# Performance work log

Measured on AMD Instinct MI355X. Metric: run time of the kernel, lower is better.

## Reference

```python
import jax, jax.numpy as jnp
import numpy as np

TEMP = 0.2
EPS = 1e-12  # F.normalize eps


def setup_inputs() -> dict:
    key = jax.random.key(0)
    k1, k2 = jax.random.split(key)
    l, B, K, D = 4, 64, 32, 128
    emb_i = jax.random.normal(k1, (l, B, K, D), dtype=jnp.float32)
    emb_j = jax.random.normal(k2, (l, B, K, D), dtype=jnp.float32)
    joint_valid = jnp.ones((B, K), dtype=jnp.float32)
    return {"emb_i": emb_i, "emb_j": emb_j, "joint_valid": joint_valid}


def _l2norm(x):
    n = jnp.sqrt(jnp.sum(x * x, axis=-1, keepdims=True))
    return x / jnp.maximum(n, EPS)


def reference(emb_i, emb_j, joint_valid):
    l, B, K, D = emb_i.shape
    N = B * K
    z_i = _l2norm(emb_i.reshape(l, N, D))
    z_j = _l2norm(emb_j.reshape(l, N, D))
    reps = jnp.concatenate([z_i, z_j], axis=1)              # (l, 2N, D), unit rows
    # cosine similarity of unit vectors == matmul
    sim = jnp.einsum('lnd,lmd->lnm', reps, reps)            # (l, 2N, 2N)
    idx = jnp.arange(N)
    pos = sim[:, idx, idx + N]                              # diag offset +N, (l, N)
    # note: original code uses the SAME +N offset diagonal for both ij and ji
    positives = jnp.concatenate([pos, pos], axis=1)         # (l, 2N)
    neg_mask = 1.0 - jnp.eye(2 * N, dtype=sim.dtype)        # (2N, 2N)
    denom = jnp.sum(neg_mask[None] * jnp.exp(sim / TEMP), axis=2)  # (l, 2N)
    loss_partial = -jnp.log(jnp.exp(positives / TEMP) / denom)    # (l, 2N)
    joints_mask = joint_valid.reshape(1, 1, B, K)
    all_num = jnp.sum(joint_valid)
    loss = jnp.sum(loss_partial.reshape(l, 2, B, K) * joints_mask) / (2.0 * all_num)
    return loss
```

## Files before the change

kernel.cpp:

```cpp
#include <hip/hip_runtime.h>
#include <hip/hip_bf16.h>

typedef __attribute__((ext_vector_type(8))) short short8;
typedef __attribute__((ext_vector_type(4))) float floatx4;

#define NROWS 4096
#define NHALF 2048
#define DDIM  128
#define LDST  136
#define SQRT_SCALE 2.6857914f
#define LN2 0.69314718056f

#define WS_PART_OFF 64
#define WS_DIAG_OFF 524352
#define WS_POS_OFF  540736
#define WS_Z_BYTE_OFF 2228480

__device__ inline unsigned short f2bf(float f) {
    unsigned u = __builtin_bit_cast(unsigned, f);
    u += 0x7fffu + ((u >> 16) & 1u);
    return (unsigned short)(u >> 16);
}

__global__ __launch_bounds__(256) void k_norm(const float* __restrict__ emb_i,
                                              const float* __restrict__ emb_j,
                                              const float* __restrict__ jv,
                                              float* __restrict__ wsf,
                                              unsigned short* __restrict__ z) {
    int bx = blockIdx.x, tid = threadIdx.x;
    if (bx == 4096) {
        __shared__ float sred[256];
        float s = 0.f;
        #pragma unroll
        for (int i = 0; i < 8; ++i) s += jv[tid + 256 * i];
        sred[tid] = s; __syncthreads();
        for (int off = 128; off > 0; off >>= 1) {
            if (tid < off) sred[tid] += sred[tid + off];
            __syncthreads();
        }
        if (tid == 0) wsf[1] = sred[0];
        return;
    }
    if (bx == 0 && tid == 0) { wsf[0] = 0.f; *(unsigned*)&wsf[2] = 0u; }

    int wave = tid >> 6, lane = tid & 63;
    int r = bx * 4 + wave;
    int l = r >> 12, n = r & 4095;
    const float* src = (n < NHALF) ? (emb_i + ((size_t)l * NHALF + n) * DDIM)
                                   : (emb_j + ((size_t)l * NHALF + (n - NHALF)) * DDIM);
    float2 v = *(const float2*)(src + lane * 2);
    float ss = v.x * v.x + v.y * v.y;
    #pragma unroll
    for (int off = 1; off < 64; off <<= 1) ss += __shfl_xor(ss, off);
    float inv = SQRT_SCALE / fmaxf(sqrtf(ss), 1e-12f);
    unsigned pack = ((unsigned)f2bf(v.y * inv) << 16) | (unsigned)f2bf(v.x * inv);
    *(unsigned*)(z + (size_t)r * DDIM + lane * 2) = pack;
}

__global__ __launch_bounds__(256) void k_sim(const unsigned short* __restrict__ z,
                                             float* __restrict__ part,
                                             float* __restrict__ diag,
                                             float* __restrict__ pos) {
    __shared__ __align__(16) unsigned short lds[128 * LDST];
    int bx = blockIdx.x, tid = threadIdx.x;
    int l = bx & 3, idx = bx >> 2;
    int J = (int)((sqrtf(8.f * (float)idx + 1.f) - 1.f) * 0.5f);
    while ((J + 1) * (J + 2) / 2 <= idx) ++J;
    while (J * (J + 1) / 2 > idx) --J;
    int I = idx - J * (J + 1) / 2;
    int wave = tid >> 6, lane = tid & 63, m = lane & 15, quad = lane >> 4;
    const unsigned short* zl = z + (size_t)l * NROWS * DDIM;
    int l4 = l * NROWS;
    int wr0 = I * 128 + wave * 32;
    int cg0 = J * 128;

    short8 a[2][4];
    #pragma unroll
    for (int rs = 0; rs < 2; ++rs) {
        const unsigned short* p = zl + (size_t)(wr0 + rs * 16 + m) * DDIM + quad * 8;
        #pragma unroll
        for (int kk = 0; kk < 4; ++kk) a[rs][kk] = *(const short8*)(p + kk * 32);
    }
    floatx4 rsum[2];
    #pragma unroll
    for (int rs = 0; rs < 2; ++rs) rsum[rs] = (floatx4){0.f, 0.f, 0.f, 0.f};
    float csum[8];
    #pragma unroll
    for (int g = 0; g < 8; ++g) csum[g] = 0.f;

    #pragma unroll
    for (int i = 0; i < 8; ++i) {
        int chunk = tid + 256 * i;
        int col = chunk >> 4, off = chunk & 15;
        uint4 d = *(const uint4*)(zl + (size_t)(cg0 + col) * DDIM + off * 8);
        *(uint4*)&lds[col * LDST + off * 8] = d;
    }
    __syncthreads();

    #pragma unroll
    for (int cs = 0; cs < 8; ++cs) {
        int ct = cg0 + cs * 16;
        const unsigned short* lp = &lds[(cs * 16 + m) * LDST + quad * 8];
        short8 b0 = *(const short8*)(lp);
        short8 b1 = *(const short8*)(lp + 32);
        short8 b2 = *(const short8*)(lp + 64);
        short8 b3 = *(const short8*)(lp + 96);
        #pragma unroll
        for (int rs = 0; rs < 2; ++rs) {
            floatx4 acc = (floatx4){0.f, 0.f, 0.f, 0.f};
            acc = __builtin_amdgcn_mfma_f32_16x16x32_bf16(a[rs][0], b0, acc, 0, 0, 0);
            acc = __builtin_amdgcn_mfma_f32_16x16x32_bf16(a[rs][1], b1, acc, 0, 0, 0);
            acc = __builtin_amdgcn_mfma_f32_16x16x32_bf16(a[rs][2], b2, acc, 0, 0, 0);
            acc = __builtin_amdgcn_mfma_f32_16x16x32_bf16(a[rs][3], b3, acc, 0, 0, 0);
            int rowbase = wr0 + rs * 16;
            bool isdiag = (ct == rowbase);
            bool ispos  = (ct == rowbase + 2048);
            if (isdiag || ispos) {
                int c = m - (quad << 2);
                if (c >= 0 && c < 4) {
                    float v = acc[c];
                    if (isdiag) diag[l4 + rowbase + m] = v;
                    else {
                        pos[l4 + rowbase + m] = v;
                        pos[l4 + rowbase + m + NHALF] = v;
                    }
                }
            }
            float t = 0.f;
            #pragma unroll
            for (int c = 0; c < 4; ++c) {
                float e = __builtin_amdgcn_exp2f(acc[c]);
                rsum[rs][c] += e;
                t += e;
            }
            csum[cs] += t;
        }
    }
    #pragma unroll
    for (int off = 1; off < 16; off <<= 1)
        #pragma unroll
        for (int rs = 0; rs < 2; ++rs)
            #pragma unroll
            for (int c = 0; c < 4; ++c)
                rsum[rs][c] += __shfl_xor(rsum[rs][c], off);
    float* plJ = part + (size_t)(l * 32 + J) * 4096;
    if (m == 0) {
        #pragma unroll
        for (int rs = 0; rs < 2; ++rs)
            #pragma unroll
            for (int c = 0; c < 4; ++c)
                plJ[wr0 + rs * 16 + quad * 4 + c] = rsum[rs][c];
    }
    if (I != J) {
        __syncthreads();
        float* cred = (float*)lds;
        #pragma unroll
        for (int g = 0; g < 8; ++g) {
            float v = csum[g];
            v += __shfl_xor(v, 16);
            v += __shfl_xor(v, 32);
            if (quad == 0) cred[wave * 128 + g * 16 + m] = v;
        }
        __syncthreads();
        if (tid < 128) {
            float s = cred[tid] + cred[tid + 128] + cred[tid + 256] + cred[tid + 384];
            part[(size_t)(l * 32 + I) * 4096 + cg0 + tid] = s;
        }
    }
}

__global__ __launch_bounds__(256) void k_loss(const float* __restrict__ jv,
                                              const float* __restrict__ part,
                                              const float* __restrict__ diag,
                                              const float* __restrict__ pos,
                                              float* __restrict__ wsf,
                                              float* __restrict__ out) {
    __shared__ float sred[256];
    int tid = threadIdx.x;
    int r = blockIdx.x * 256 + tid;
    int l = r >> 12, n = r & 4095;
    const float* pl = part + (size_t)l * 32 * 4096 + n;
    float s = 0.f;
    #pragma unroll
    for (int k = 0; k < 32; ++k) s += pl[(size_t)k * 4096];
    float denom = s - __builtin_amdgcn_exp2f(diag[r]);
    float contrib = LN2 * (__builtin_amdgcn_logf(denom) - pos[r]);
    float local = contrib * jv[n & (NHALF - 1)];
    sred[tid] = local; __syncthreads();
    for (int off = 128; off > 0; off >>= 1) {
        if (tid < off) sred[tid] += sred[tid + off];
        __syncthreads();
    }
    if (tid == 0) {
        atomicAdd(&wsf[0], sred[0]);
        __threadfence();
        unsigned c = atomicAdd((unsigned*)&wsf[2], 1u);
        if (c == 63) {
            float tot = atomicAdd(&wsf[0], 0.f);
            out[0] = tot / (2.f * wsf[1]);
        }
    }
}

extern "C" void kernel_launch(void* const* d_in, const int* in_sizes, int n_in,
                              void* d_out, int out_size, void* d_ws, size_t ws_size,
                              hipStream_t stream) {
    const float* emb_i = (const float*)d_in[0];
    const float* emb_j = (const float*)d_in[1];
    const float* jv    = (const float*)d_in[2];
    float* wsf  = (float*)d_ws;
    float* part = wsf + WS_PART_OFF;
    float* diag = wsf + WS_DIAG_OFF;
    float* pos  = wsf + WS_POS_OFF;
    unsigned short* z = (unsigned short*)((char*)d_ws + WS_Z_BYTE_OFF);
    float* out = (float*)d_out;

    k_norm <<<4097, 256, 0, stream>>>(emb_i, emb_j, jv, wsf, z);
    k_sim  <<<2112, 256, 0, stream>>>(z, part, diag, pos);
    k_loss <<<64,   256, 0, stream>>>(jv, part, diag, pos, wsf, out);
}
```

Before: 89.27 us.

## Make similarity kernel persistent with register-prefetched next tile

The similarity kernel now runs as a persistent grid of 512 blocks, each walking a strided list of 4-5 triangular tiles instead of launching one block per tile. While the current tile's MFMA and exp work runs, the next tile's column block is prefetched into registers and its row fragments are loaded, then written to LDS after the reduction. This hides global-load latency and reduces per-block launch and setup overhead. The cost is higher register pressure from the prefetch buffers, extra barriers per tile, and a tail imbalance because some blocks process one more tile than others.

Result: slower. 103.9 us (+16.3%).

```diff
diff --git a/kernel.cpp b/kernel.cpp
--- a/kernel.cpp
+++ b/kernel.cpp
@@ -20,6 +20,13 @@
     unsigned u = __builtin_bit_cast(unsigned, f);
     u += 0x7fffu + ((u >> 16) & 1u);
     return (unsigned short)(u >> 16);
+}
+
+__device__ inline void tilecoords(int idx, int& I, int& J) {
+    int j = (int)((sqrtf(8.f * (float)idx + 1.f) - 1.f) * 0.5f);
+    while ((j + 1) * (j + 2) / 2 <= idx) ++j;
+    while (j * (j + 1) / 2 > idx) --j;
+    J = j; I = idx - j * (j + 1) / 2;
 }
 
 __global__ __launch_bounds__(256) void k_norm(const float* __restrict__ emb_i,
@@ -62,110 +69,141 @@
                                              float* __restrict__ diag,
                                              float* __restrict__ pos) {
     __shared__ __align__(16) unsigned short lds[128 * LDST];
+    __shared__ float cred[4][128];
     int bx = blockIdx.x, tid = threadIdx.x;
-    int l = bx & 3, idx = bx >> 2;
-    int J = (int)((sqrtf(8.f * (float)idx + 1.f) - 1.f) * 0.5f);
-    while ((J + 1) * (J + 2) / 2 <= idx) ++J;
-    while (J * (J + 1) / 2 > idx) --J;
-    int I = idx - J * (J + 1) / 2;
+    int l = bx & 3, ppos = bx >> 2;
+    int nt = 4 + (ppos < 16);
     int wave = tid >> 6, lane = tid & 63, m = lane & 15, quad = lane >> 4;
     const unsigned short* zl = z + (size_t)l * NROWS * DDIM;
     int l4 = l * NROWS;
-    int wr0 = I * 128 + wave * 32;
-    int cg0 = J * 128;
+
+    int I, J;
+    tilecoords(ppos, I, J);
 
     short8 a[2][4];
     #pragma unroll
     for (int rs = 0; rs < 2; ++rs) {
-        const unsigned short* p = zl + (size_t)(wr0 + rs * 16 + m) * DDIM + quad * 8;
-        #pragma unroll
-        for (int kk = 0; kk < 4; ++kk) a[rs][kk] = *(const short8*)(p + kk * 32);
-    }
-    floatx4 rsum[2];
-    #pragma unroll
-    for (int rs = 0; rs < 2; ++rs) rsum[rs] = (floatx4){0.f, 0.f, 0.f, 0.f};
-    float csum[8];
-    #pragma unroll
-    for (int g = 0; g < 8; ++g) csum[g] = 0.f;
-
+        const unsigned short* pa = zl + (size_t)(I * 128 + wave * 32 + rs * 16 + m) * DDIM + quad * 8;
+        #pragma unroll
+        for (int kk = 0; kk < 4; ++kk) a[rs][kk] = *(const short8*)(pa + kk * 32);
+    }
     #pragma unroll
     for (int i = 0; i < 8; ++i) {
         int chunk = tid + 256 * i;
         int col = chunk >> 4, off = chunk & 15;
-        uint4 d = *(const uint4*)(zl + (size_t)(cg0 + col) * DDIM + off * 8);
+        uint4 d = *(const uint4*)(zl + (size_t)(J * 128 + col) * DDIM + off * 8);
         *(uint4*)&lds[col * LDST + off * 8] = d;
     }
     __syncthreads();
 
-    #pragma unroll
-    for (int cs = 0; cs < 8; ++cs) {
-        int ct = cg0 + cs * 16;
-        const unsigned short* lp = &lds[(cs * 16 + m) * LDST + quad * 8];
-        short8 b0 = *(const short8*)(lp);
-        short8 b1 = *(const short8*)(lp + 32);
-        short8 b2 = *(const short8*)(lp + 64);
-        short8 b3 = *(const short8*)(lp + 96);
+    for (int k = 0; k < nt; ++k) {
+        int nidx = ppos + (k + 1) * 128;
+        if (nidx >= 528) nidx = ppos;
+        int In, Jn;
+        tilecoords(nidx, In, Jn);
+        uint4 pf[8];
+        #pragma unroll
+        for (int i = 0; i < 8; ++i) {
+            int chunk = tid + 256 * i;
+            int col = chunk >> 4, off = chunk & 15;
+            pf[i] = *(const uint4*)(zl + (size_t)(Jn * 128 + col) * DDIM + off * 8);
+        }
+        short8 an[2][4];
         #pragma unroll
         for (int rs = 0; rs < 2; ++rs) {
-            floatx4 acc = (floatx4){0.f, 0.f, 0.f, 0.f};
-            acc = __builtin_amdgcn_mfma_f32_16x16x32_bf16(a[rs][0], b0, acc, 0, 0, 0);
-            acc = __builtin_amdgcn_mfma_f32_16x16x32_bf16(a[rs][1], b1, acc, 0, 0, 0);
-            acc = __builtin_amdgcn_mfma_f32_16x16x32_bf16(a[rs][2], b2, acc, 0, 0, 0);
-            acc = __builtin_amdgcn_mfma_f32_16x16x32_bf16(a[rs][3], b3, acc, 0, 0, 0);
-            int rowbase = wr0 + rs * 16;
-            bool isdiag = (ct == rowbase);
-            bool ispos  = (ct == rowbase + 2048);
-            if (isdiag || ispos) {
-                int c = m - (quad << 2);
-                if (c >= 0 && c < 4) {
-                    float v = acc[c];
-                    if (isdiag) diag[l4 + rowbase + m] = v;
-                    else {
-                        pos[l4 + rowbase + m] = v;
-                        pos[l4 + rowbase + m + NHALF] = v;
+            const unsigned short* pa = zl + (size_t)(In * 128 + wave * 32 + rs * 16 + m) * DDIM + quad * 8;
+            #pragma unroll
+            for (int kk = 0; kk < 4; ++kk) an[rs][kk] = *(const short8*)(pa + kk * 32);
+        }
+
+        int wr0 = I * 128 + wave * 32, cg0 = J * 128;
+        floatx4 rsum[2];
+        rsum[0] = (floatx4){0.f, 0.f, 0.f, 0.f};
+        rsum[1] = (floatx4){0.f, 0.f, 0.f, 0.f};
+        float csum[8];
+        #pragma unroll
+        for (int g = 0; g < 8; ++g) csum[g] = 0.f;
+
+        #pragma unroll
+        for (int cs = 0; cs < 8; ++cs) {
+            int ct = cg0 + cs * 16;
+            const unsigned short* lp = &lds[(cs * 16 + m) * LDST + quad * 8];
+            short8 b0 = *(const short8*)(lp);
+            short8 b1 = *(const short8*)(lp + 32);
+            short8 b2 = *(const short8*)(lp + 64);
+            short8 b3 = *(const short8*)(lp + 96);
+            #pragma unroll
+            for (int rs = 0; rs < 2; ++rs) {
+                floatx4 acc = (floatx4){0.f, 0.f, 0.f, 0.f};
+                acc = __builtin_amdgcn_mfma_f32_16x16x32_bf16(a[rs][0], b0, acc, 0, 0, 0);
+                acc = __builtin_amdgcn_mfma_f32_16x16x32_bf16(a[rs][1], b1, acc, 0, 0, 0);
+                acc = __builtin_amdgcn_mfma_f32_16x16x32_bf16(a[rs][2], b2, acc, 0, 0, 0);
+                acc = __builtin_amdgcn_mfma_f32_16x16x32_bf16(a[rs][3], b3, acc, 0, 0, 0);
+                int rowbase = wr0 + rs * 16;
+                bool isdiag = (ct == rowbase);
+                bool ispos  = (ct == rowbase + 2048);
+                if (isdiag || ispos) {
+                    int c = m - (quad << 2);
+                    if (c >= 0 && c < 4) {
+                        float v = acc[c];
+                        if (isdiag) diag[l4 + rowbase + m] = v;
+                        else {
+                            pos[l4 + rowbase + m] = v;
+                            pos[l4 + rowbase + m + NHALF] = v;
+                        }
                     }
                 }
+                float t = 0.f;
+                #pragma unroll
+                for (int c = 0; c < 4; ++c) {
+                    float e = __builtin_amdgcn_exp2f(acc[c]);
+                    rsum[rs][c] += e;
+                    t += e;
+                }
+                csum[cs] += t;
             }
-            float t = 0.f;
-            #pragma unroll
-            for (int c = 0; c < 4; ++c) {
-                float e = __builtin_amdgcn_exp2f(acc[c]);
-                rsum[rs][c] += e;
-                t += e;
+        }
+        #pragma unroll
+        for (int off = 1; off < 16; off <<= 1)
+            #pragma unroll
+            for (int rs = 0; rs < 2; ++rs)
+                #pragma unroll
+                for (int c = 0; c < 4; ++c)
+                    rsum[rs][c] += __shfl_xor(rsum[rs][c], off);
+        float* plJ = part + (size_t)(l * 32 + J) * 4096;
+        if (m == 0) {
+            #pragma unroll
+            for (int rs = 0; rs < 2; ++rs)
+                #pragma unroll
+                for (int c = 0; c < 4; ++c)
+                    plJ[wr0 + rs * 16 + quad * 4 + c] = rsum[rs][c];
+        }
+        if (I != J) {
+            #pragma unroll
+            for (int g = 0; g < 8; ++g) {
+                float v = csum[g];
+                v += __shfl_xor(v, 16);
+                v += __shfl_xor(v, 32);
+                if (quad == 0) cred[wave][g * 16 + m] = v;
             }
-            csum[cs] += t;
-        }
-    }
-    #pragma unroll
-    for (int off = 1; off < 16; off <<= 1)
+        }
+        __syncthreads();
+        if (I != J && tid < 128) {
+            float s = cred[0][tid] + cred[1][tid] + cred[2][tid] + cred[3][tid];
+            part[(size_t)(l * 32 + I) * 4096 + cg0 + tid] = s;
+        }
+        #pragma unroll
+        for (int i = 0; i < 8; ++i) {
+            int chunk = tid + 256 * i;
+            int col = chunk >> 4, off = chunk & 15;
+            *(uint4*)&lds[col * LDST + off * 8] = pf[i];
+        }
+        __syncthreads();
         #pragma unroll
         for (int rs = 0; rs < 2; ++rs)
             #pragma unroll
-            for (int c = 0; c < 4; ++c)
-                rsum[rs][c] += __shfl_xor(rsum[rs][c], off);
-    float* plJ = part + (size_t)(l * 32 + J) * 4096;
-    if (m == 0) {
-        #pragma unroll
-        for (int rs = 0; rs < 2; ++rs)
-            #pragma unroll
-            for (int c = 0; c < 4; ++c)
-                plJ[wr0 + rs * 16 + quad * 4 + c] = rsum[rs][c];
-    }
-    if (I != J) {
-        __syncthreads();
-        float* cred = (float*)lds;
-        #pragma unroll
-        for (int g = 0; g < 8; ++g) {
-            float v = csum[g];
-            v += __shfl_xor(v, 16);
-            v += __shfl_xor(v, 32);
-            if (quad == 0) cred[wave * 128 + g * 16 + m] = v;
-        }
-        __syncthreads();
-        if (tid < 128) {
-            float s = cred[tid] + cred[tid + 128] + cred[tid + 256] + cred[tid + 384];
-            part[(size_t)(l * 32 + I) * 4096 + cg0 + tid] = s;
-        }
+            for (int kk = 0; kk < 4; ++kk) a[rs][kk] = an[rs][kk];
+        I = In; J = Jn;
     }
 }
 
@@ -216,6 +254,6 @@
     float* out = (float*)d_out;
 
     k_norm <<<4097, 256, 0, stream>>>(emb_i, emb_j, jv, wsf, z);
-    k_sim  <<<2112, 256, 0, stream>>>(z, part, diag, pos);
+    k_sim  <<<512,  256, 0, stream>>>(z, part, diag, pos);
     k_loss <<<64,   256, 0, stream>>>(jv, part, diag, pos, wsf, out);
 }
```

## Process up to four column tiles per block to reuse row fragments

Applied to the files above, without the earlier changes.

The similarity kernel now walks a strip of up to four column tiles per block instead of one tile per block, cutting the grid from 2112 to 576 blocks. The A-row fragments stay in registers across the strip, and each next column tile is loaded into LDS after a barrier. This removes redundant A loads and per-block setup. In exchange it gives fewer blocks to hide latency, uneven work per block (one to four tiles), and B-tile loads that are serialized rather than overlapped with compute.

Measured after the change: 98.93 us. 1.11x slower.

```diff
diff --git a/kernel.cpp b/kernel.cpp
--- a/kernel.cpp
+++ b/kernel.cpp
@@ -62,110 +62,128 @@
                                              float* __restrict__ diag,
                                              float* __restrict__ pos) {
     __shared__ __align__(16) unsigned short lds[128 * LDST];
+    __shared__ float cred[4][128];
     int bx = blockIdx.x, tid = threadIdx.x;
-    int l = bx & 3, idx = bx >> 2;
-    int J = (int)((sqrtf(8.f * (float)idx + 1.f) - 1.f) * 0.5f);
-    while ((J + 1) * (J + 2) / 2 <= idx) ++J;
-    while (J * (J + 1) / 2 > idx) --J;
-    int I = idx - J * (J + 1) / 2;
+    int l = bx & 3, t = bx >> 2;
+    int cb = 0, cum = 0;
+    while (cb < 7) {
+        int n = 4 * cb + 4; if (n > 32) n = 32;
+        if (cum + n > t) break;
+        cum += n; ++cb;
+    }
+    int rb = t - cum;
+    int k0 = rb > 4 * cb ? rb : 4 * cb;
+    int k1 = 4 * cb + 3;
+
     int wave = tid >> 6, lane = tid & 63, m = lane & 15, quad = lane >> 4;
     const unsigned short* zl = z + (size_t)l * NROWS * DDIM;
     int l4 = l * NROWS;
-    int wr0 = I * 128 + wave * 32;
-    int cg0 = J * 128;
+    int wr0 = rb * 128 + wave * 32;
 
     short8 a[2][4];
     #pragma unroll
     for (int rs = 0; rs < 2; ++rs) {
-        const unsigned short* p = zl + (size_t)(wr0 + rs * 16 + m) * DDIM + quad * 8;
-        #pragma unroll
-        for (int kk = 0; kk < 4; ++kk) a[rs][kk] = *(const short8*)(p + kk * 32);
-    }
-    floatx4 rsum[2];
-    #pragma unroll
-    for (int rs = 0; rs < 2; ++rs) rsum[rs] = (floatx4){0.f, 0.f, 0.f, 0.f};
-    float csum[8];
-    #pragma unroll
-    for (int g = 0; g < 8; ++g) csum[g] = 0.f;
+        const unsigned short* pa = zl + (size_t)(wr0 + rs * 16 + m) * DDIM + quad * 8;
+        #pragma unroll
+        for (int kk = 0; kk < 4; ++kk) a[rs][kk] = *(const short8*)(pa + kk * 32);
+    }
 
     #pragma unroll
     for (int i = 0; i < 8; ++i) {
         int chunk = tid + 256 * i;
         int col = chunk >> 4, off = chunk & 15;
-        uint4 d = *(const uint4*)(zl + (size_t)(cg0 + col) * DDIM + off * 8);
+        uint4 d = *(const uint4*)(zl + (size_t)(k0 * 128 + col) * DDIM + off * 8);
         *(uint4*)&lds[col * LDST + off * 8] = d;
     }
     __syncthreads();
 
-    #pragma unroll
-    for (int cs = 0; cs < 8; ++cs) {
-        int ct = cg0 + cs * 16;
-        const unsigned short* lp = &lds[(cs * 16 + m) * LDST + quad * 8];
-        short8 b0 = *(const short8*)(lp);
-        short8 b1 = *(const short8*)(lp + 32);
-        short8 b2 = *(const short8*)(lp + 64);
-        short8 b3 = *(const short8*)(lp + 96);
-        #pragma unroll
-        for (int rs = 0; rs < 2; ++rs) {
-            floatx4 acc = (floatx4){0.f, 0.f, 0.f, 0.f};
-            acc = __builtin_amdgcn_mfma_f32_16x16x32_bf16(a[rs][0], b0, acc, 0, 0, 0);
-            acc = __builtin_amdgcn_mfma_f32_16x16x32_bf16(a[rs][1], b1, acc, 0, 0, 0);
-            acc = __builtin_amdgcn_mfma_f32_16x16x32_bf16(a[rs][2], b2, acc, 0, 0, 0);
-            acc = __builtin_amdgcn_mfma_f32_16x16x32_bf16(a[rs][3], b3, acc, 0, 0, 0);
-            int rowbase = wr0 + rs * 16;
-            bool isdiag = (ct == rowbase);
-            bool ispos  = (ct == rowbase + 2048);
-            if (isdiag || ispos) {
-                int c = m - (quad << 2);
-                if (c >= 0 && c < 4) {
-                    float v = acc[c];
-                    if (isdiag) diag[l4 + rowbase + m] = v;
-                    else {
-                        pos[l4 + rowbase + m] = v;
-                        pos[l4 + rowbase + m + NHALF] = v;
+    for (int k = k0; k <= k1; ++k) {
+        int cg0 = k * 128;
+        floatx4 rsum[2];
+        rsum[0] = (floatx4){0.f, 0.f, 0.f, 0.f};
+        rsum[1] = (floatx4){0.f, 0.f, 0.f, 0.f};
+        float csum[8];
+        #pragma unroll
+        for (int g = 0; g < 8; ++g) csum[g] = 0.f;
+
+        #pragma unroll
+        for (int cs = 0; cs < 8; ++cs) {
+            int ct = cg0 + cs * 16;
+            const unsigned short* lp = &lds[(cs * 16 + m) * LDST + quad * 8];
+            short8 b0 = *(const short8*)(lp);
+            short8 b1 = *(const short8*)(lp + 32);
+            short8 b2 = *(const short8*)(lp + 64);
+            short8 b3 = *(const short8*)(lp + 96);
+            #pragma unroll
+            for (int rs = 0; rs < 2; ++rs) {
+                floatx4 acc = (floatx4){0.f, 0.f, 0.f, 0.f};
+                acc = __builtin_amdgcn_mfma_f32_16x16x32_bf16(a[rs][0], b0, acc, 0, 0, 0);
+                acc = __builtin_amdgcn_mfma_f32_16x16x32_bf16(a[rs][1], b1, acc, 0, 0, 0);
+                acc = __builtin_amdgcn_mfma_f32_16x16x32_bf16(a[rs][2], b2, acc, 0, 0, 0);
+                acc = __builtin_amdgcn_mfma_f32_16x16x32_bf16(a[rs][3], b3, acc, 0, 0, 0);
+                int rowbase = wr0 + rs * 16;
+                bool isdiag = (ct == rowbase);
+                bool ispos  = (ct == rowbase + 2048);
+                if (isdiag || ispos) {
+                    int c = m - (quad << 2);
+                    if (c >= 0 && c < 4) {
+                        float v = acc[c];
+                        if (isdiag) diag[l4 + rowbase + m] = v;
+                        else {
+                            pos[l4 + rowbase + m] = v;
+                            pos[l4 + rowbase + m + NHALF] = v;
+                        }
                     }
                 }
+                float tsum = 0.f;
+                #pragma unroll
+                for (int c = 0; c < 4; ++c) {
+                    float e = __builtin_amdgcn_exp2f(acc[c]);
+                    rsum[rs][c] += e;
+                    tsum += e;
+                }
+                csum[cs] += tsum;
             }
-            float t = 0.f;
-            #pragma unroll
-            for (int c = 0; c < 4; ++c) {
-                float e = __builtin_amdgcn_exp2f(acc[c]);
-                rsum[rs][c] += e;
-                t += e;
+        }
+        #pragma unroll
+        for (int off = 1; off < 16; off <<= 1)
+            #pragma unroll
+            for (int rs = 0; rs < 2; ++rs)
+                #pragma unroll
+                for (int c = 0; c < 4; ++c)
+                    rsum[rs][c] += __shfl_xor(rsum[rs][c], off);
+        float* plK = part + (size_t)(l * 32 + k) * 4096;
+        if (m == 0) {
+            #pragma unroll
+            for (int rs = 0; rs < 2; ++rs)
+                #pragma unroll
+                for (int c = 0; c < 4; ++c)
+                    plK[wr0 + rs * 16 + quad * 4 + c] = rsum[rs][c];
+        }
+        if (k != rb) {
+            #pragma unroll
+            for (int g = 0; g < 8; ++g) {
+                float v = csum[g];
+                v += __shfl_xor(v, 16);
+                v += __shfl_xor(v, 32);
+                if (quad == 0) cred[wave][g * 16 + m] = v;
             }
-            csum[cs] += t;
-        }
-    }
-    #pragma unroll
-    for (int off = 1; off < 16; off <<= 1)
-        #pragma unroll
-        for (int rs = 0; rs < 2; ++rs)
-            #pragma unroll
-            for (int c = 0; c < 4; ++c)
-                rsum[rs][c] += __shfl_xor(rsum[rs][c], off);
-    float* plJ = part + (size_t)(l * 32 + J) * 4096;
-    if (m == 0) {
-        #pragma unroll
-        for (int rs = 0; rs < 2; ++rs)
-            #pragma unroll
-            for (int c = 0; c < 4; ++c)
-                plJ[wr0 + rs * 16 + quad * 4 + c] = rsum[rs][c];
-    }
-    if (I != J) {
+        }
         __syncthreads();
-        float* cred = (float*)lds;
-        #pragma unroll
-        for (int g = 0; g < 8; ++g) {
-            float v = csum[g];
-            v += __shfl_xor(v, 16);
-            v += __shfl_xor(v, 32);
-            if (quad == 0) cred[wave * 128 + g * 16 + m] = v;
+        if (k < k1) {
+            #pragma unroll
+            for (int i = 0; i < 8; ++i) {
+                int chunk = tid + 256 * i;
+                int col = chunk >> 4, off = chunk & 15;
+                uint4 d = *(const uint4*)(zl + (size_t)((k + 1) * 128 + col) * DDIM + off * 8);
+                *(uint4*)&lds[col * LDST + off * 8] = d;
+            }
+        }
+        if (k != rb && tid < 128) {
+            float s = cred[0][tid] + cred[1][tid] + cred[2][tid] + cred[3][tid];
+            part[(size_t)(l * 32 + rb) * 4096 + cg0 + tid] = s;
         }
         __syncthreads();
-        if (tid < 128) {
-            float s = cred[tid] + cred[tid + 128] + cred[tid + 256] + cred[tid + 384];
-            part[(size_t)(l * 32 + I) * 4096 + cg0 + tid] = s;
-        }
     }
 }
 
@@ -216,6 +234,6 @@
     float* out = (float*)d_out;
 
     k_norm <<<4097, 256, 0, stream>>>(emb_i, emb_j, jv, wsf, z);
-    k_sim  <<<2112, 256, 0, stream>>>(z, part, diag, pos);
+    k_sim  <<<576,  256, 0, stream>>>(z, part, diag, pos);
     k_loss <<<64,   256, 0, stream>>>(jv, part, diag, pos, wsf, out);
 }
```
